# Performance work log

Measured on AMD Instinct MI355X. Metric: run time of the kernel, lower is better.

## Reference

```python
import jax, jax.numpy as jnp
import numpy as np

D_MODEL = 1024
N_HEADS = 16
D_HEAD = D_MODEL // N_HEADS
D_FF = 4 * D_MODEL
SEQ = 2048
BATCH = 4
EPS = 1e-5


def setup_inputs() -> dict:
    key = jax.random.key(0)
    ks = jax.random.split(key, 12)
    s = 0.02
    return {
        "x": jax.random.normal(ks[0], (BATCH, SEQ, D_MODEL), dtype=jnp.float32),
        "ln1_g": jnp.ones((D_MODEL,), jnp.float32),
        "ln1_b": jnp.zeros((D_MODEL,), jnp.float32),
        "wq": jax.random.normal(ks[1], (N_HEADS, D_MODEL, D_HEAD), jnp.float32) * s,
        "bq": jnp.zeros((N_HEADS, D_HEAD), jnp.float32),
        "wk": jax.random.normal(ks[2], (N_HEADS, D_MODEL, D_HEAD), jnp.float32) * s,
        "bk": jnp.zeros((N_HEADS, D_HEAD), jnp.float32),
        "wv": jax.random.normal(ks[3], (N_HEADS, D_MODEL, D_HEAD), jnp.float32) * s,
        "bv": jnp.zeros((N_HEADS, D_HEAD), jnp.float32),
        "wp": jax.random.normal(ks[4], (D_MODEL, D_MODEL), jnp.float32) * s,
        "bp": jnp.zeros((D_MODEL,), jnp.float32),
        "ln2_g": jnp.ones((D_MODEL,), jnp.float32),
        "ln2_b": jnp.zeros((D_MODEL,), jnp.float32),
        "w1": jax.random.normal(ks[5], (D_MODEL, D_FF), jnp.float32) * s,
        "b1": jnp.zeros((D_FF,), jnp.float32),
        "w2": jax.random.normal(ks[6], (D_FF, D_MODEL), jnp.float32) * s,
        "b2": jnp.zeros((D_MODEL,), jnp.float32),
    }


def _layer_norm(x, g, b):
    mu = jnp.mean(x, axis=-1, keepdims=True)
    var = jnp.mean(jnp.square(x - mu), axis=-1, keepdims=True)
    return (x - mu) * jax.lax.rsqrt(var + EPS) * g + b


def _block(x, ln1_g, ln1_b, wq, bq, wk, bk, wv, bv, wp, bp,
           ln2_g, ln2_b, w1, b1, w2, b2):
    B, S, D = x.shape
    # --- pre-LN multi-head causal self-attention ---
    xn = _layer_norm(x, ln1_g, ln1_b)
    q = jnp.einsum('bsd,hde->bhse', xn, wq) + bq[None, :, None, :]
    k = jnp.einsum('bsd,hde->bhse', xn, wk) + bk[None, :, None, :]
    v = jnp.einsum('bsd,hde->bhse', xn, wv) + bv[None, :, None, :]
    scores = jnp.einsum('bhse,bhte->bhst', q, k) / np.sqrt(D_HEAD).astype(np.float32)
    causal = jnp.tril(jnp.ones((S, S), dtype=bool))
    scores = jnp.where(causal[None, None], scores, jnp.float32(-jnp.inf))
    attn = jax.nn.softmax(scores, axis=-1)
    o = jnp.einsum('bhst,bhte->bhse', attn, v)          # [B,H,S,Dh]
    o = o.transpose(0, 2, 1, 3).reshape(B, S, D)         # concat heads
    x = x + o @ wp + bp
    # --- pre-LN feedforward ---
    xn2 = _layer_norm(x, ln2_g, ln2_b)
    h = jax.nn.relu(xn2 @ w1 + b1)
    x = x + h @ w2 + b2
    return x


def reference(x, ln1_g, ln1_b, wq, bq, wk, bk, wv, bv, wp, bp,
              ln2_g, ln2_b, w1, b1, w2, b2):
    return _block(x, ln1_g, ln1_b, wq, bq, wk, bk, wv, bv, wp, bp,
                  ln2_g, ln2_b, w1, b1, w2, b2)
```

## Files before the change

### kernel.cpp

```cpp
#include <hip/hip_runtime.h>
#include <hip/hip_bf16.h>

#define D_MODEL 1024
#define N_HEADS 16
#define D_HEAD  64
#define D_FF    4096
#define SEQ     2048
#define BATCH   4
#define NROWS   (BATCH * SEQ)

typedef __attribute__((ext_vector_type(8))) short short8;
typedef __attribute__((ext_vector_type(4))) float f32x4;

#define EXP2(x) exp2f(x)

static __device__ __forceinline__ ushort f2bf(float x) {
  __hip_bfloat16 h = __float2bfloat16(x);
  return *reinterpret_cast<ushort*>(&h);
}

static __device__ __forceinline__ void gl_lds16(const ushort* g, ushort* l) {
  __builtin_amdgcn_global_load_lds(
      (const __attribute__((address_space(1))) void*)g,
      (__attribute__((address_space(3))) void*)l, 16, 0, 0);
}

__global__ __launch_bounds__(256) void transpose_pack_b(
    const float* __restrict__ in, ushort* __restrict__ out,
    int K, int N, size_t in_bs, size_t out_bs) {
  in  += (size_t)blockIdx.z * in_bs;
  out += (size_t)blockIdx.z * out_bs;
  __shared__ float tile[32][33];
  int n0 = blockIdx.x * 32, k0 = blockIdx.y * 32;
  int tx = threadIdx.x, ty = threadIdx.y;
#pragma unroll
  for (int i = 0; i < 32; i += 8)
    tile[ty + i][tx] = in[(size_t)(k0 + ty + i) * N + n0 + tx];
  __syncthreads();
#pragma unroll
  for (int i = 0; i < 32; i += 8)
    out[(size_t)(n0 + ty + i) * K + k0 + tx] = f2bf(tile[tx][ty + i]);
}

__global__ __launch_bounds__(256) void transpose_v(
    const ushort* __restrict__ v, ushort* __restrict__ vt) {
  const int s0 = blockIdx.x * 64;
  const int bh = blockIdx.y, bb = bh >> 4, hh = bh & 15;
  __shared__ ushort tile[64][66];
  const ushort* src = v + (size_t)bb * SEQ * D_MODEL + (size_t)hh * 64;
  const int tx = threadIdx.x;
#pragma unroll
  for (int i = threadIdx.y; i < 64; i += 4)
    tile[i][tx] = src[(size_t)(s0 + i) * D_MODEL + tx];
  __syncthreads();
  ushort* dst = vt + (size_t)bh * 64 * SEQ + s0;
#pragma unroll
  for (int d = threadIdx.y; d < 64; d += 4)
    dst[(size_t)d * SEQ + tx] = tile[tx][d];
}

__global__ __launch_bounds__(256) void ln_kernel(
    const float* __restrict__ x, const float* __restrict__ g,
    const float* __restrict__ b, ushort* __restrict__ out) {
  int row = blockIdx.x, t = threadIdx.x;
  const float4 v = *(const float4*)(x + (size_t)row * D_MODEL + t * 4);
  float s  = v.x + v.y + v.z + v.w;
  float ss = v.x * v.x + v.y * v.y + v.z * v.z + v.w * v.w;
#pragma unroll
  for (int off = 1; off < 64; off <<= 1) {
    s  += __shfl_xor(s, off, 64);
    ss += __shfl_xor(ss, off, 64);
  }
  __shared__ float rs_[4], rss_[4];
  int w = t >> 6;
  if ((t & 63) == 0) { rs_[w] = s; rss_[w] = ss; }
  __syncthreads();
  s  = rs_[0] + rs_[1] + rs_[2] + rs_[3];
  ss = rss_[0] + rss_[1] + rss_[2] + rss_[3];
  float mu  = s * (1.0f / D_MODEL);
  float var = ss * (1.0f / D_MODEL) - mu * mu;
  float rstd = rsqrtf(var + 1e-5f);
  float4 gg = *(const float4*)(g + t * 4);
  float4 bb = *(const float4*)(b + t * 4);
  ushort4 r;
  r.x = f2bf((v.x - mu) * rstd * gg.x + bb.x);
  r.y = f2bf((v.y - mu) * rstd * gg.y + bb.y);
  r.z = f2bf((v.z - mu) * rstd * gg.z + bb.z);
  r.w = f2bf((v.w - mu) * rstd * gg.w + bb.w);
  *(ushort4*)(out + (size_t)row * D_MODEL + t * 4) = r;
}

template <int MODE>
__global__ __launch_bounds__(512, 2) void gemm256(
    const ushort* __restrict__ A, const ushort* __restrict__ BT,
    int M, int N, int K,
    const float* __restrict__ bias0, const float* __restrict__ bias1,
    const float* __restrict__ bias2,
    void* __restrict__ out0, void* __restrict__ out1, void* __restrict__ out2) {
  __shared__ __align__(16) ushort As[2][256 * 64];
  __shared__ __align__(16) ushort Bs[2][256 * 64];
  const int gx = N >> 8;
  const int nwg = gx * (M >> 8);
  const int cpx = nwg >> 3;
  const int tile = (blockIdx.x & 7) * cpx + (blockIdx.x >> 3);
  const int bn = tile % gx, bm = tile / gx;
  const int t = threadIdx.x, lane = t & 63, w = t >> 6;
  const int wr = w >> 2, wc = w & 3;
  const int l16 = lane & 15, l4 = lane >> 4;

  const ushort* Ab = A + (size_t)(bm * 256) * K;
  const ushort* Bb = BT + (size_t)(bn * 256) * K;

  int srow[4], scol[4];
#pragma unroll
  for (int i = 0; i < 4; ++i) {
    int c = i * 512 + t;
    srow[i] = c >> 3;
    scol[i] = 8 * ((c & 7) ^ ((c >> 3) & 7));
  }

  f32x4 acc[8][4] = {};
  int cur = 0;
  const int nk = K >> 6;

#pragma unroll
  for (int i = 0; i < 4; ++i) {
    gl_lds16(&Ab[(size_t)srow[i] * K + scol[i]], (ushort*)&As[0][(i * 512 + w * 64) * 8]);
    gl_lds16(&Bb[(size_t)srow[i] * K + scol[i]], (ushort*)&Bs[0][(i * 512 + w * 64) * 8]);
  }
  asm volatile("s_waitcnt vmcnt(0)" ::: "memory");
  __syncthreads();

  for (int kt = 0; kt < nk; ++kt) {
    if (kt + 1 < nk) {
      const int k0n = (kt + 1) << 6;
#pragma unroll
      for (int i = 0; i < 4; ++i) {
        gl_lds16(&Ab[(size_t)srow[i] * K + k0n + scol[i]], (ushort*)&As[cur ^ 1][(i * 512 + w * 64) * 8]);
        gl_lds16(&Bb[(size_t)srow[i] * K + k0n + scol[i]], (ushort*)&Bs[cur ^ 1][(i * 512 + w * 64) * 8]);
      }
    }
    const ushort* As_ = As[cur];
    const ushort* Bs_ = Bs[cur];
    short8 bfr[4][2];
#pragma unroll
    for (int n = 0; n < 4; ++n) {
      const int row = wc * 64 + n * 16 + l16;
      const int sw = (row & 7) * 8;
      bfr[n][0] = *(const short8*)&Bs_[row * 64 + ((l4 * 8) ^ sw)];
      bfr[n][1] = *(const short8*)&Bs_[row * 64 + ((l4 * 8 + 32) ^ sw)];
    }
#pragma unroll
    for (int m = 0; m < 8; ++m) {
      const int row = wr * 128 + m * 16 + l16;
      const int sw = (row & 7) * 8;
      short8 a0 = *(const short8*)&As_[row * 64 + ((l4 * 8) ^ sw)];
      short8 a1 = *(const short8*)&As_[row * 64 + ((l4 * 8 + 32) ^ sw)];
#pragma unroll
      for (int n = 0; n < 4; ++n) {
        acc[m][n] = __builtin_amdgcn_mfma_f32_16x16x32_bf16(a0, bfr[n][0], acc[m][n], 0, 0, 0);
        acc[m][n] = __builtin_amdgcn_mfma_f32_16x16x32_bf16(a1, bfr[n][1], acc[m][n], 0, 0, 0);
      }
    }
    asm volatile("s_waitcnt vmcnt(0)" ::: "memory");
    __syncthreads();
    cur ^= 1;
  }

  const int row0 = bm * 256 + wr * 128, col0 = bn * 256 + wc * 64;
#pragma unroll
  for (int m = 0; m < 8; ++m) {
#pragma unroll
    for (int n = 0; n < 4; ++n) {
      const int col = col0 + n * 16 + l16;
      if (MODE == 0) {
        const int which = col >> 10;
        const int c = col & 1023;
        const float* bp_ = (which == 0) ? bias0 : (which == 1) ? bias1 : bias2;
        ushort* op = (which == 0) ? (ushort*)out0 : (which == 1) ? (ushort*)out1 : (ushort*)out2;
        const float scale = (which == 0) ? 0.125f * 1.44269504f : 1.0f;
#pragma unroll
        for (int i = 0; i < 4; ++i) {
          const int row = row0 + m * 16 + l4 * 4 + i;
          op[(size_t)row * D_MODEL + c] = f2bf((acc[m][n][i] + bp_[c]) * scale);
        }
      } else {
#pragma unroll
        for (int i = 0; i < 4; ++i) {
          const int row = row0 + m * 16 + l4 * 4 + i;
          const float val = fmaxf(acc[m][n][i] + bias0[col], 0.0f);
          ((ushort*)out0)[(size_t)row * D_FF + col] = f2bf(val);
        }
      }
    }
  }
}

template <int MODE>
__global__ __launch_bounds__(256) void gemm128(
    const ushort* __restrict__ A, const ushort* __restrict__ BT,
    int M, int N, int K,
    const float* __restrict__ bias0, const float* __restrict__ resid,
    float* __restrict__ out0) {
  __shared__ __align__(16) ushort As[128 * 32];
  __shared__ __align__(16) ushort Bs[128 * 32];
  const int gx = N >> 7;
  const int nwg = gx * (M >> 7);
  const int cpx = nwg >> 3;
  const int tile = (blockIdx.x & 7) * cpx + (blockIdx.x >> 3);
  const int bn = tile % gx, bm = tile / gx;

  const int t = threadIdx.x, lane = t & 63, w = t >> 6;
  const int wr = w >> 1, wc = w & 1;
  const int l16 = lane & 15, l4 = lane >> 4;

  const int c0 = t, c1 = 256 + t;
  const int ar0 = c0 >> 2, ae0 = (c0 & 3) * 8;
  const int ar1 = c1 >> 2, ae1 = (c1 & 3) * 8;
  const ushort* Ab = A + (size_t)(bm * 128) * K;
  const ushort* Bb = BT + (size_t)(bn * 128) * K;
  ushort* AsW0 = &As[(0 * 256 + w * 64) * 8];
  ushort* AsW1 = &As[(1 * 256 + w * 64) * 8];
  ushort* BsW0 = &Bs[(0 * 256 + w * 64) * 8];
  ushort* BsW1 = &Bs[(1 * 256 + w * 64) * 8];

  f32x4 acc[4][4] = {};

  for (int k0 = 0; k0 < K; k0 += 32) {
    __syncthreads();
    gl_lds16(&Ab[(size_t)ar0 * K + k0 + ae0], AsW0);
    gl_lds16(&Ab[(size_t)ar1 * K + k0 + ae1], AsW1);
    gl_lds16(&Bb[(size_t)ar0 * K + k0 + ae0], BsW0);
    gl_lds16(&Bb[(size_t)ar1 * K + k0 + ae1], BsW1);
    __syncthreads();
    short8 a[4], b[4];
#pragma unroll
    for (int m = 0; m < 4; ++m)
      a[m] = *(const short8*)&As[(wr * 64 + m * 16 + l16) * 32 + l4 * 8];
#pragma unroll
    for (int n = 0; n < 4; ++n)
      b[n] = *(const short8*)&Bs[(wc * 64 + n * 16 + l16) * 32 + l4 * 8];
#pragma unroll
    for (int m = 0; m < 4; ++m)
#pragma unroll
      for (int n = 0; n < 4; ++n)
        acc[m][n] = __builtin_amdgcn_mfma_f32_16x16x32_bf16(a[m], b[n], acc[m][n], 0, 0, 0);
  }

  const int row0 = bm * 128 + wr * 64, col0 = bn * 128 + wc * 64;
#pragma unroll
  for (int m = 0; m < 4; ++m) {
#pragma unroll
    for (int n = 0; n < 4; ++n) {
      const int col = col0 + n * 16 + l16;
#pragma unroll
      for (int i = 0; i < 4; ++i) {
        const int row = row0 + m * 16 + l4 * 4 + i;
        const size_t idx = (size_t)row * D_MODEL + col;
        out0[idx] = acc[m][n][i] + bias0[col] + resid[idx];
      }
    }
  }
}

__global__ __launch_bounds__(256) void attn4_kernel(
    const ushort* __restrict__ Q, const ushort* __restrict__ Km,
    const ushort* __restrict__ Vt, ushort* __restrict__ O) {
  const int b = blockIdx.x;
  const int bh = (b & 7) * 8 + ((b >> 3) & 7);
  const int qt = 15 - (b >> 6);
  const int bb = bh >> 4, hh = bh & 15;
  const int t = threadIdx.x, lane = t & 63, w = t >> 6;
  const int l16 = lane & 15, l4 = lane >> 4;
  const size_t base  = (size_t)bb * SEQ * D_MODEL + (size_t)hh * 64;
  const size_t vbase = (size_t)bh * 64 * SEQ;
  const int qb = qt * 128 + w * 32;

  __shared__ __align__(16) ushort Ks[2][64 * 64];
  __shared__ __align__(16) ushort Vs[2][64 * 64];
  __shared__ __align__(16) ushort Pw[4][32 * 64];
  ushort* myP = &Pw[w][0];

  short8 qf[2][2];
#pragma unroll
  for (int qj = 0; qj < 2; ++qj)
#pragma unroll
    for (int dk = 0; dk < 2; ++dk)
      qf[qj][dk] = *(const short8*)&Q[base + (size_t)(qb + qj * 16 + l16) * D_MODEL + dk * 32 + l4 * 8];

  f32x4 oacc[4][2] = {};
  float m_i[2] = {-1e30f, -1e30f}, l_i[2] = {0.0f, 0.0f};

  const int nt = qt * 2 + 2;

#define STAGE(ktile, buf) do {                                                     \
    const int kv0_ = (ktile) * 64;                                                 \
    _Pragma("unroll")                                                              \
    for (int i_ = 0; i_ < 2; ++i_) {                                               \
      const int g_ = i_ * 256 + t;                                                 \
      const int row_ = g_ >> 3;                                                    \
      const int c8_ = ((g_ & 7) ^ (row_ & 7)) * 8;                                 \
      gl_lds16(&Km[base + (size_t)(kv0_ + row_) * D_MODEL + c8_],                  \
               (ushort*)&Ks[buf][(i_ * 256 + w * 64) * 8]);                        \
      gl_lds16(&Vt[vbase + (size_t)row_ * SEQ + kv0_ + c8_],                       \
               (ushort*)&Vs[buf][(i_ * 256 + w * 64) * 8]);                        \
    }                                                                              \
  } while (0)

  STAGE(0, 0);
  asm volatile("s_waitcnt vmcnt(0)" ::: "memory");
  __syncthreads();

  int cur = 0;
  for (int kt = 0; kt < nt; ++kt) {
    const int kv0 = kt * 64;
    if (kt + 1 < nt) STAGE(kt + 1, cur ^ 1);

    const bool active = (kv0 <= qb + 31);
    if (active) {
      const ushort* Kc = Ks[cur];
      const ushort* Vc = Vs[cur];

      f32x4 sacc[2][4] = {};
#pragma unroll
      for (int n = 0; n < 4; ++n) {
        const int r = n * 16 + l16;
        const int rs = r * 8, rx = r & 7;
#pragma unroll
        for (int dk = 0; dk < 2; ++dk) {
          short8 ak = *(const short8*)&Kc[(rs + ((dk * 4 + l4) ^ rx)) * 8];
          sacc[0][n] = __builtin_amdgcn_mfma_f32_16x16x32_bf16(ak, qf[0][dk], sacc[0][n], 0, 0, 0);
          sacc[1][n] = __builtin_amdgcn_mfma_f32_16x16x32_bf16(ak, qf[1][dk], sacc[1][n], 0, 0, 0);
        }
      }

      const bool diag = (kv0 + 63 > qb);
#pragma unroll
      for (int qj = 0; qj < 2; ++qj) {
        const int qq = qb + qj * 16 + l16;
        const int ql = qj * 16 + l16;
        const int psw = (ql & 7) * 8;
        if (diag) {
#pragma unroll
          for (int n = 0; n < 4; ++n)
#pragma unroll
            for (int i = 0; i < 4; ++i) {
              const int kv = kv0 + n * 16 + l4 * 4 + i;
              if (kv > qq) sacc[qj][n][i] = -1e30f;
            }
        }
        float mx = -1e30f;
#pragma unroll
        for (int n = 0; n < 4; ++n)
#pragma unroll
          for (int i = 0; i < 4; ++i) mx = fmaxf(mx, sacc[qj][n][i]);
        mx = fmaxf(mx, __shfl_xor(mx, 16, 64));
        mx = fmaxf(mx, __shfl_xor(mx, 32, 64));

        if (__any(mx > m_i[qj] + 8.0f)) {
          const float mnew = fmaxf(m_i[qj], mx);
          const float alpha = EXP2(m_i[qj] - mnew);
          m_i[qj] = mnew;
          l_i[qj] *= alpha;
#pragma unroll
          for (int nd = 0; nd < 4; ++nd)
#pragma unroll
            for (int i = 0; i < 4; ++i) oacc[nd][qj][i] *= alpha;
        }

        float lsum = 0.0f;
#pragma unroll
        for (int n = 0; n < 4; ++n) {
          const float p0 = EXP2(sacc[qj][n][0] - m_i[qj]);
          const float p1 = EXP2(sacc[qj][n][1] - m_i[qj]);
          const float p2 = EXP2(sacc[qj][n][2] - m_i[qj]);
          const float p3 = EXP2(sacc[qj][n][3] - m_i[qj]);
          lsum += p0 + p1 + p2 + p3;
          ushort4 pk;
          pk.x = f2bf(p0); pk.y = f2bf(p1); pk.z = f2bf(p2); pk.w = f2bf(p3);
          *(ushort4*)&myP[ql * 64 + ((n * 16 + l4 * 4) ^ psw)] = pk;
        }
        lsum += __shfl_xor(lsum, 16, 64);
        lsum += __shfl_xor(lsum, 32, 64);
        l_i[qj] += lsum;
      }

#pragma unroll
      for (int kk = 0; kk < 2; ++kk) {
        short8 bp[2];
#pragma unroll
        for (int qj = 0; qj < 2; ++qj) {
          const int ql = qj * 16 + l16;
          bp[qj] = *(const short8*)&myP[ql * 64 + ((kk * 32 + l4 * 8) ^ ((ql & 7) * 8))];
        }
#pragma unroll
        for (int nd = 0; nd < 4; ++nd) {
          const int r = nd * 16 + l16;
          short8 av = *(const short8*)&Vc[(r * 8 + ((kk * 4 + l4) ^ (r & 7))) * 8];
          oacc[nd][0] = __builtin_amdgcn_mfma_f32_16x16x32_bf16(av, bp[0], oacc[nd][0], 0, 0, 0);
          oacc[nd][1] = __builtin_amdgcn_mfma_f32_16x16x32_bf16(av, bp[1], oacc[nd][1], 0, 0, 0);
        }
      }
    }

    asm volatile("s_waitcnt vmcnt(0)" ::: "memory");
    __syncthreads();
    cur ^= 1;
  }
#undef STAGE

#pragma unroll
  for (int qj = 0; qj < 2; ++qj) {
    const int qq = qb + qj * 16 + l16;
    const float inv = 1.0f / l_i[qj];
#pragma unroll
    for (int nd = 0; nd < 4; ++nd) {
      ushort4 r;
      r.x = f2bf(oacc[nd][qj][0] * inv);
      r.y = f2bf(oacc[nd][qj][1] * inv);
      r.z = f2bf(oacc[nd][qj][2] * inv);
      r.w = f2bf(oacc[nd][qj][3] * inv);
      *(ushort4*)&O[base + (size_t)qq * D_MODEL + nd * 16 + l4 * 4] = r;
    }
  }
}

extern "C" void kernel_launch(void* const* d_in, const int* in_sizes, int n_in,
                              void* d_out, int out_size, void* d_ws, size_t ws_size,
                              hipStream_t stream) {
  const float* x    = (const float*)d_in[0];
  const float* ln1g = (const float*)d_in[1];
  const float* ln1b = (const float*)d_in[2];
  const float* wq   = (const float*)d_in[3];
  const float* bq   = (const float*)d_in[4];
  const float* wk   = (const float*)d_in[5];
  const float* bk   = (const float*)d_in[6];
  const float* wv   = (const float*)d_in[7];
  const float* bv   = (const float*)d_in[8];
  const float* wp   = (const float*)d_in[9];
  const float* bp   = (const float*)d_in[10];
  const float* ln2g = (const float*)d_in[11];
  const float* ln2b = (const float*)d_in[12];
  const float* w1   = (const float*)d_in[13];
  const float* b1   = (const float*)d_in[14];
  const float* w2   = (const float*)d_in[15];
  const float* b2   = (const float*)d_in[16];
  float* out = (float*)d_out;

  char* base = (char*)d_ws;
  size_t off = 0;
  auto alloc = [&](size_t bytes) -> void* {
    void* r = base + off;
    off += (bytes + 255) & ~(size_t)255;
    return r;
  };
  ushort* WqkvT = (ushort*)alloc((size_t)3 * D_MODEL * D_MODEL * 2);
  ushort* WpT   = (ushort*)alloc((size_t)D_MODEL * D_MODEL * 2);
  ushort* W1T   = (ushort*)alloc((size_t)D_FF * D_MODEL * 2);
  ushort* W2T   = (ushort*)alloc((size_t)D_MODEL * D_FF * 2);
  ushort* xn    = (ushort*)alloc((size_t)NROWS * D_MODEL * 2);
  ushort* q     = (ushort*)alloc((size_t)NROWS * D_MODEL * 2);
  ushort* k     = (ushort*)alloc((size_t)NROWS * D_MODEL * 2);
  ushort* v     = (ushort*)alloc((size_t)NROWS * D_MODEL * 2);
  ushort* o     = (ushort*)alloc((size_t)NROWS * D_MODEL * 2);
  float*  x2    = (float*) alloc((size_t)NROWS * D_MODEL * 4);
  ushort* xn2   = (ushort*)alloc((size_t)NROWS * D_MODEL * 2);
  ushort* hbuf  = (ushort*)alloc((size_t)NROWS * D_FF * 2);
  ushort* vt = xn;

  dim3 tb(32, 8);
  transpose_pack_b<<<dim3(2, 32, 16), tb, 0, stream>>>(wq, WqkvT + (size_t)0 * D_MODEL * D_MODEL,
      D_MODEL, D_HEAD, (size_t)D_MODEL * D_HEAD, (size_t)D_HEAD * D_MODEL);
  transpose_pack_b<<<dim3(2, 32, 16), tb, 0, stream>>>(wk, WqkvT + (size_t)1 * D_MODEL * D_MODEL,
      D_MODEL, D_HEAD, (size_t)D_MODEL * D_HEAD, (size_t)D_HEAD * D_MODEL);
  transpose_pack_b<<<dim3(2, 32, 16), tb, 0, stream>>>(wv, WqkvT + (size_t)2 * D_MODEL * D_MODEL,
      D_MODEL, D_HEAD, (size_t)D_MODEL * D_HEAD, (size_t)D_HEAD * D_MODEL);
  transpose_pack_b<<<dim3(32, 32, 1), tb, 0, stream>>>(wp, WpT, D_MODEL, D_MODEL, 0, 0);
  transpose_pack_b<<<dim3(128, 32, 1), tb, 0, stream>>>(w1, W1T, D_MODEL, D_FF, 0, 0);
  transpose_pack_b<<<dim3(32, 128, 1), tb, 0, stream>>>(w2, W2T, D_FF, D_MODEL, 0, 0);

  ln_kernel<<<NROWS, 256, 0, stream>>>(x, ln1g, ln1b, xn);
  gemm256<0><<<dim3((NROWS / 256) * (3 * D_MODEL / 256)), 512, 0, stream>>>(
      xn, WqkvT, NROWS, 3 * D_MODEL, D_MODEL, bq, bk, bv, q, k, v);
  transpose_v<<<dim3(SEQ / 64, BATCH * N_HEADS), dim3(64, 4), 0, stream>>>(v, vt);
  attn4_kernel<<<1024, 256, 0, stream>>>(q, k, vt, o);
  gemm128<1><<<dim3((NROWS / 128) * (D_MODEL / 128)), 256, 0, stream>>>(
      o, WpT, NROWS, D_MODEL, D_MODEL, bp, x, x2);
  ln_kernel<<<NROWS, 256, 0, stream>>>(x2, ln2g, ln2b, xn2);
  gemm256<2><<<dim3((NROWS / 256) * (D_FF / 256)), 512, 0, stream>>>(
      xn2, W1T, NROWS, D_FF, D_MODEL, b1, nullptr, nullptr, hbuf, nullptr, nullptr);
  gemm128<3><<<dim3((NROWS / 128) * (D_MODEL / 128)), 256, 0, stream>>>(
      hbuf, W2T, NROWS, D_MODEL, D_FF, b2, x2, out);
}
```

Measured before the change: 421.1 us.

## Replace 128x128 output GEMMs with double-buffered swizzled 256x128 tile kernel

The projection and FFN-down GEMMs now use a 256x128 tile with 512 threads, a BK of 64, double-buffered LDS with prefetch of the next K slice, and XOR-swizzled LDS layout. This aims to overlap global loads with MFMA work, halve the barriers per K, reduce LDS bank conflicts and increase operand reuse. The trade-offs are larger LDS use (96KB) and fewer workgroups (256), which may limit occupancy and leave some CUs idle.

Result: faster. 400.0 us (-5.0%).

```diff
diff --git a/kernel.cpp b/kernel.cpp
--- a/kernel.cpp
+++ b/kernel.cpp
@@ -196,58 +196,84 @@
   }
 }
 
-template <int MODE>
-__global__ __launch_bounds__(256) void gemm128(
+__global__ __launch_bounds__(512, 2) void gemm256x128(
     const ushort* __restrict__ A, const ushort* __restrict__ BT,
     int M, int N, int K,
     const float* __restrict__ bias0, const float* __restrict__ resid,
     float* __restrict__ out0) {
-  __shared__ __align__(16) ushort As[128 * 32];
-  __shared__ __align__(16) ushort Bs[128 * 32];
+  __shared__ __align__(16) ushort As[2][256 * 64];
+  __shared__ __align__(16) ushort Bs[2][128 * 64];
   const int gx = N >> 7;
-  const int nwg = gx * (M >> 7);
+  const int nwg = gx * (M >> 8);
   const int cpx = nwg >> 3;
   const int tile = (blockIdx.x & 7) * cpx + (blockIdx.x >> 3);
   const int bn = tile % gx, bm = tile / gx;
-
   const int t = threadIdx.x, lane = t & 63, w = t >> 6;
   const int wr = w >> 1, wc = w & 1;
   const int l16 = lane & 15, l4 = lane >> 4;
 
-  const int c0 = t, c1 = 256 + t;
-  const int ar0 = c0 >> 2, ae0 = (c0 & 3) * 8;
-  const int ar1 = c1 >> 2, ae1 = (c1 & 3) * 8;
-  const ushort* Ab = A + (size_t)(bm * 128) * K;
+  const ushort* Ab = A + (size_t)(bm * 256) * K;
   const ushort* Bb = BT + (size_t)(bn * 128) * K;
-  ushort* AsW0 = &As[(0 * 256 + w * 64) * 8];
-  ushort* AsW1 = &As[(1 * 256 + w * 64) * 8];
-  ushort* BsW0 = &Bs[(0 * 256 + w * 64) * 8];
-  ushort* BsW1 = &Bs[(1 * 256 + w * 64) * 8];
+
+  int srow[4], scol[4];
+#pragma unroll
+  for (int i = 0; i < 4; ++i) {
+    int c = i * 512 + t;
+    srow[i] = c >> 3;
+    scol[i] = 8 * ((c & 7) ^ ((c >> 3) & 7));
+  }
 
   f32x4 acc[4][4] = {};
-
-  for (int k0 = 0; k0 < K; k0 += 32) {
+  int cur = 0;
+  const int nk = K >> 6;
+
+#pragma unroll
+  for (int i = 0; i < 4; ++i)
+    gl_lds16(&Ab[(size_t)srow[i] * K + scol[i]], (ushort*)&As[0][(i * 512 + w * 64) * 8]);
+#pragma unroll
+  for (int i = 0; i < 2; ++i)
+    gl_lds16(&Bb[(size_t)srow[i] * K + scol[i]], (ushort*)&Bs[0][(i * 512 + w * 64) * 8]);
+  asm volatile("s_waitcnt vmcnt(0)" ::: "memory");
+  __syncthreads();
+
+  for (int kt = 0; kt < nk; ++kt) {
+    if (kt + 1 < nk) {
+      const int k0n = (kt + 1) << 6;
+#pragma unroll
+      for (int i = 0; i < 4; ++i)
+        gl_lds16(&Ab[(size_t)srow[i] * K + k0n + scol[i]], (ushort*)&As[cur ^ 1][(i * 512 + w * 64) * 8]);
+#pragma unroll
+      for (int i = 0; i < 2; ++i)
+        gl_lds16(&Bb[(size_t)srow[i] * K + k0n + scol[i]], (ushort*)&Bs[cur ^ 1][(i * 512 + w * 64) * 8]);
+    }
+    const ushort* As_ = As[cur];
+    const ushort* Bs_ = Bs[cur];
+    short8 bfr[4][2];
+#pragma unroll
+    for (int n = 0; n < 4; ++n) {
+      const int row = wc * 64 + n * 16 + l16;
+      const int sw = (row & 7) * 8;
+      bfr[n][0] = *(const short8*)&Bs_[row * 64 + ((l4 * 8) ^ sw)];
+      bfr[n][1] = *(const short8*)&Bs_[row * 64 + ((l4 * 8 + 32) ^ sw)];
+    }
+#pragma unroll
+    for (int m = 0; m < 4; ++m) {
+      const int row = wr * 64 + m * 16 + l16;
+      const int sw = (row & 7) * 8;
+      short8 a0 = *(const short8*)&As_[row * 64 + ((l4 * 8) ^ sw)];
+      short8 a1 = *(const short8*)&As_[row * 64 + ((l4 * 8 + 32) ^ sw)];
+#pragma unroll
+      for (int n = 0; n < 4; ++n) {
+        acc[m][n] = __builtin_amdgcn_mfma_f32_16x16x32_bf16(a0, bfr[n][0], acc[m][n], 0, 0, 0);
+        acc[m][n] = __builtin_amdgcn_mfma_f32_16x16x32_bf16(a1, bfr[n][1], acc[m][n], 0, 0, 0);
+      }
+    }
+    asm volatile("s_waitcnt vmcnt(0)" ::: "memory");
     __syncthreads();
-    gl_lds16(&Ab[(size_t)ar0 * K + k0 + ae0], AsW0);
-    gl_lds16(&Ab[(size_t)ar1 * K + k0 + ae1], AsW1);
-    gl_lds16(&Bb[(size_t)ar0 * K + k0 + ae0], BsW0);
-    gl_lds16(&Bb[(size_t)ar1 * K + k0 + ae1], BsW1);
-    __syncthreads();
-    short8 a[4], b[4];
-#pragma unroll
-    for (int m = 0; m < 4; ++m)
-      a[m] = *(const short8*)&As[(wr * 64 + m * 16 + l16) * 32 + l4 * 8];
-#pragma unroll
-    for (int n = 0; n < 4; ++n)
-      b[n] = *(const short8*)&Bs[(wc * 64 + n * 16 + l16) * 32 + l4 * 8];
-#pragma unroll
-    for (int m = 0; m < 4; ++m)
-#pragma unroll
-      for (int n = 0; n < 4; ++n)
-        acc[m][n] = __builtin_amdgcn_mfma_f32_16x16x32_bf16(a[m], b[n], acc[m][n], 0, 0, 0);
-  }
-
-  const int row0 = bm * 128 + wr * 64, col0 = bn * 128 + wc * 64;
+    cur ^= 1;
+  }
+
+  const int row0 = bm * 256 + wr * 64, col0 = bn * 128 + wc * 64;
 #pragma unroll
   for (int m = 0; m < 4; ++m) {
 #pragma unroll
@@ -484,11 +510,11 @@
       xn, WqkvT, NROWS, 3 * D_MODEL, D_MODEL, bq, bk, bv, q, k, v);
   transpose_v<<<dim3(SEQ / 64, BATCH * N_HEADS), dim3(64, 4), 0, stream>>>(v, vt);
   attn4_kernel<<<1024, 256, 0, stream>>>(q, k, vt, o);
-  gemm128<1><<<dim3((NROWS / 128) * (D_MODEL / 128)), 256, 0, stream>>>(
+  gemm256x128<<<dim3((NROWS / 256) * (D_MODEL / 128)), 512, 0, stream>>>(
       o, WpT, NROWS, D_MODEL, D_MODEL, bp, x, x2);
   ln_kernel<<<NROWS, 256, 0, stream>>>(x2, ln2g, ln2b, xn2);
   gemm256<2><<<dim3((NROWS / 256) * (D_FF / 256)), 512, 0, stream>>>(
       xn2, W1T, NROWS, D_FF, D_MODEL, b1, nullptr, nullptr, hbuf, nullptr, nullptr);
-  gemm128<3><<<dim3((NROWS / 128) * (D_MODEL / 128)), 256, 0, stream>>>(
+  gemm256x128<<<dim3((NROWS / 256) * (D_MODEL / 128)), 512, 0, stream>>>(
       hbuf, W2T, NROWS, D_MODEL, D_FF, b2, x2, out);
 }
```
